# Performance work log

Hardware: AMD Instinct MI355X
Metric: run time of the kernel (lower is better)

The kernel has to match this reference:

```python
import jax, jax.numpy as jnp
import numpy as np

N_QUBITS = 14
N_LAYERS = 3
BATCH = 256


def _apply_1q(state, U, q, n):
    # state: (B, 2^n) flat; apply 2x2 gate U on qubit q.
    # U: (2,2) shared or (B,2,2) per-sample.
    B = state.shape[0]
    s = state.reshape(B, 2 ** q, 2, 2 ** (n - 1 - q))
    if U.ndim == 3:
        s = jnp.einsum('bij,bajc->baic', U, s)
    else:
        s = jnp.einsum('ij,bajc->baic', U, s)
    return s.reshape(B, -1)


def _apply_cnot(state, c, t, n):
    # CNOT: |c, t> -> |c, t xor c>. Flip target axis on the control=1 block.
    B = state.shape[0]
    a, b = (c, t) if c < t else (t, c)
    s = state.reshape(B, 2 ** a, 2, 2 ** (b - a - 1), 2, 2 ** (n - 1 - b))
    c_ax = 2 if c < t else 4
    t_ax = 4 if c < t else 2
    s0 = jax.lax.index_in_dim(s, 0, axis=c_ax, keepdims=False)
    s1 = jax.lax.index_in_dim(s, 1, axis=c_ax, keepdims=False)
    t_ax2 = t_ax if t_ax < c_ax else t_ax - 1
    s1 = jnp.flip(s1, axis=t_ax2)
    s = jnp.stack([s0, s1], axis=c_ax)
    return s.reshape(B, -1)


def _circuit(x, weights, n, L):
    # angles constrained to (-pi, pi) as in the torch wrapper
    angles = jnp.tanh(x) * jnp.float32(np.pi)  # (B, n)
    B = x.shape[0]
    state = jnp.zeros((B, 2 ** n), jnp.complex64).at[:, 0].set(1.0)
    # AngleEmbedding with RY rotations (per-sample gate matrices)
    for q in range(n):
        th = angles[:, q] * 0.5
        c, s = jnp.cos(th), jnp.sin(th)
        U = jnp.stack([jnp.stack([c, -s], -1), jnp.stack([s, c], -1)], -2)
        state = _apply_1q(state, U.astype(jnp.complex64), q, n)
    # BasicEntanglerLayers: per layer, RX(w) on each wire then CNOT ring
    for l in range(L):
        for q in range(n):
            th = weights[l, q] * 0.5
            c = jnp.cos(th).astype(jnp.complex64)
            s = jnp.sin(th).astype(jnp.complex64)
            mis = jnp.complex64(-1j) * s
            U = jnp.stack([jnp.stack([c, mis]), jnp.stack([mis, c])])
            state = _apply_1q(state, U, q, n)
        num_cnots = n if n > 2 else (1 if n == 2 else 0)
        for q in range(num_cnots):
            state = _apply_cnot(state, q, (q + 1) % n, n)
    # <Z_q> = P(q=0) - P(q=1)
    p = (jnp.abs(state) ** 2).reshape((B,) + (2,) * n)  # float32 probs
    expvals = []
    for q in range(n):
        pq = jnp.sum(p, axis=tuple(a for a in range(1, n + 1) if a != q + 1))
        expvals.append(pq[:, 0] - pq[:, 1])
    return jnp.stack(expvals, axis=-1)  # (B, n)


def setup_inputs() -> dict:
    key = jax.random.key(0)
    kx, kw = jax.random.split(key)
    x = jax.random.normal(kx, (BATCH, N_QUBITS), jnp.float32)
    # TorchLayer default init for BasicEntanglerLayers: uniform in [0, 2*pi)
    weights = jax.random.uniform(kw, (N_LAYERS, N_QUBITS), jnp.float32, 0.0, 2.0 * np.pi)
    return {"x": x, "weights": weights}


def reference(x, weights):
    return _circuit(x, weights, N_QUBITS, N_LAYERS)
```

## Files before the change

### kernel.cpp

```cpp
#include <hip/hip_runtime.h>
#include <math.h>

#define NQ 14
#define DIM (1 << NQ)
#define NT 512
#define TA 32
#define NW (NT / 64)
#define PDIM (DIM + DIM / 32)

template <int J> struct IC { static constexpr int v = J; };
template <int N, typename F>
__device__ __forceinline__ void sfor(F&& f) {
    if constexpr (N > 0) { sfor<N - 1>(f); f(IC<N - 1>{}); }
}

typedef float cf2 __attribute__((ext_vector_type(2)));

__device__ __forceinline__ cf2 pk_mul_s_swapneg(cf2 cs, cf2 a) {
    cf2 t;
    asm("v_pk_mul_f32 %0, %1, %2 op_sel:[1,1] op_sel_hi:[1,0] neg_hi:[0,1]"
        : "=v"(t) : "v"(cs), "v"(a));
    return t;
}
__device__ __forceinline__ cf2 pk_fma_c(cf2 cs, cf2 a, cf2 b) {
    cf2 d;
    asm("v_pk_fma_f32 %0, %1, %2, %3 op_sel:[0,0,0] op_sel_hi:[0,1,1]"
        : "=v"(d) : "v"(cs), "v"(a), "v"(b));
    return d;
}

struct St {
    cf2 a0, a1, a2, a3, a4, a5, a6, a7, a8, a9, a10, a11, a12, a13, a14, a15,
        a16, a17, a18, a19, a20, a21, a22, a23, a24, a25, a26, a27, a28, a29, a30, a31;
};
template <int J> __device__ __forceinline__ cf2& amp(St& s);
#define AMP_GET(J) template <> __device__ __forceinline__ cf2& amp<J>(St& s) { return s.a##J; }
AMP_GET(0)  AMP_GET(1)  AMP_GET(2)  AMP_GET(3)  AMP_GET(4)  AMP_GET(5)  AMP_GET(6)  AMP_GET(7)
AMP_GET(8)  AMP_GET(9)  AMP_GET(10) AMP_GET(11) AMP_GET(12) AMP_GET(13) AMP_GET(14) AMP_GET(15)
AMP_GET(16) AMP_GET(17) AMP_GET(18) AMP_GET(19) AMP_GET(20) AMP_GET(21) AMP_GET(22) AMP_GET(23)
AMP_GET(24) AMP_GET(25) AMP_GET(26) AMP_GET(27) AMP_GET(28) AMP_GET(29) AMP_GET(30) AMP_GET(31)

__host__ __device__ constexpr int pad(int idx) { return idx + (idx >> 5); }

template <int P0, int P1, int P2, int P3, int P4>
struct Tile5 {
    static constexpr int PMASK = (1 << P0) | (1 << P1) | (1 << P2) | (1 << P3) | (1 << P4);
    static __device__ __forceinline__ int base_idx(int t) {
        int idx = 0, tb = 0;
#pragma unroll
        for (int p = 0; p < NQ; ++p)
            if (!((PMASK >> p) & 1)) { idx |= ((t >> tb) & 1) << p; ++tb; }
        return idx;
    }
    static constexpr int off(int j) {
        return ((j & 1) << P0) | (((j >> 1) & 1) << P1) | (((j >> 2) & 1) << P2) |
               (((j >> 3) & 1) << P3) | (((j >> 4) & 1) << P4);
    }
    static constexpr int poff(int j) { return pad(off(j)); }
};

using TT1 = Tile5<9, 10, 11, 12, 13>;
using TT2 = Tile5<4, 5, 6, 7, 8>;
using TT3 = Tile5<13, 0, 1, 2, 3>;

template <class T>
__device__ __forceinline__ void load_tile(const cf2* s, int pb, St& st) {
    sfor<TA>([&](auto jc) {
        constexpr int j0 = decltype(jc)::v;
        constexpr int j = (j0 >> 1) | ((j0 & 1) << 4);
        amp<j>(st) = s[pb + T::poff(j)];
    });
}
template <class T>
__device__ __forceinline__ void load_tile_fold(const cf2* s, int pbLo, int pbHi, St& st) {
    sfor<TA>([&](auto jc) {
        constexpr int j0 = decltype(jc)::v;
        constexpr int j = (j0 >> 1) | ((j0 & 1) << 4);
        amp<j>(st) = s[((j & 16) ? pbHi : pbLo) + T::poff(j)];
    });
}
template <class T, int HI>
__device__ __forceinline__ void store_half(cf2* s, int pb, St& st) {
    sfor<TA>([&](auto jc) {
        constexpr int j = decltype(jc)::v;
        if constexpr ((j >> 4) == HI) s[pb + T::poff(j)] = amp<j>(st);
    });
}

template <int LB>
__device__ __forceinline__ void g_rx(St& st, cf2 cs) {
    sfor<TA>([&](auto jc) {
        constexpr int j = decltype(jc)::v;
        if constexpr (!(j & (1 << LB))) {
            constexpr int k = j | (1 << LB);
            cf2 aj = amp<j>(st), ak = amp<k>(st);
            amp<j>(st) = pk_fma_c(cs, aj, pk_mul_s_swapneg(cs, ak));
            amp<k>(st) = pk_fma_c(cs, ak, pk_mul_s_swapneg(cs, aj));
        }
    });
}
template <int LB, int HI>
__device__ __forceinline__ void g_rx_h(St& st, cf2 cs) {
    sfor<TA>([&](auto jc) {
        constexpr int j = decltype(jc)::v;
        if constexpr (!(j & (1 << LB)) && ((j >> 4) == HI)) {
            constexpr int k = j | (1 << LB);
            cf2 aj = amp<j>(st), ak = amp<k>(st);
            amp<j>(st) = pk_fma_c(cs, aj, pk_mul_s_swapneg(cs, ak));
            amp<k>(st) = pk_fma_c(cs, ak, pk_mul_s_swapneg(cs, aj));
        }
    });
}
template <int LC, int LT, int HI>
__device__ __forceinline__ void g_cnot_h(St& st) {
    sfor<TA>([&](auto jc) {
        constexpr int j = decltype(jc)::v;
        if constexpr (((j >> LC) & 1) && !((j >> LT) & 1) && ((j >> 4) == HI)) {
            constexpr int k = j | (1 << LT);
            cf2 t = amp<j>(st);
            amp<j>(st) = amp<k>(st);
            amp<k>(st) = t;
        }
    });
}

__device__ __forceinline__ cf2 cmul(cf2 a, cf2 b) {
    cf2 r; r.x = a.x * b.x - a.y * b.y; r.y = a.x * b.y + a.y * b.x; return r;
}
__device__ __forceinline__ cf2 v_of(cf2 ry, cf2 rx, int b) {
    cf2 r;
    r.x = b ? rx.x * ry.y : rx.x * ry.x;
    r.y = b ? -(rx.y * ry.x) : -(rx.y * ry.y);
    return r;
}

__global__ void __launch_bounds__(NT) qsim_kernel(const float* __restrict__ x,
                                                  const float* __restrict__ w,
                                                  float* __restrict__ out) {
    __shared__ cf2 sSt[PDIM];
    __shared__ cf2 sCS[56];
    __shared__ float sRed[NW][NQ];

    const int tid = threadIdx.x;
    const int b = blockIdx.x;

    if (tid < 14) {
        float th = tanhf(x[b * NQ + tid]) * 1.57079632679489662f;
        cf2 v; v.x = cosf(th); v.y = sinf(th);
        sCS[tid] = v;
    } else if (tid < 56) {
        float th = w[tid - 14] * 0.5f;
        cf2 v; v.x = cosf(th); v.y = sinf(th);
        sCS[tid] = v;
    }

    const int pbT1 = pad(TT1::base_idx(tid));
    const int pbT2 = pad(TT2::base_idx(tid));
    const int pbT3 = pad(TT3::base_idx(tid));
    const int d2 = ((tid >> 4) & 1) ? 264 : 0;
    const int pbT2lo = pbT2 + d2, pbT2hi = pbT2 - d2;
    const int d3 = (tid & 1) ? 8 : 0;
    const int pbT3lo = pbT3 + d3, pbT3hi = pbT3 - d3;

    __syncthreads();

    St st;

    {
        const int t0 = tid & 1,        t1 = (tid >> 1) & 1, t2 = (tid >> 2) & 1,
                  t3 = (tid >> 3) & 1, t4 = (tid >> 4) & 1, t5 = (tid >> 5) & 1,
                  t6 = (tid >> 6) & 1, t7 = (tid >> 7) & 1, t8 = (tid >> 8) & 1;
        const int b6 = t7 ^ t8, b7 = t6 ^ t7, b8 = t5 ^ t6, b9 = t4 ^ t5;
        const int b10 = t3 ^ t4, b11 = t2 ^ t3, b12 = t1 ^ t2, b13 = t0 ^ t1;
        cf2 Pref = v_of(sCS[6], sCS[20], b6);
        Pref = cmul(Pref, v_of(sCS[7],  sCS[21], b7));
        Pref = cmul(Pref, v_of(sCS[8],  sCS[22], b8));
        Pref = cmul(Pref, v_of(sCS[9],  sCS[23], b9));
        Pref = cmul(Pref, v_of(sCS[10], sCS[24], b10));
        Pref = cmul(Pref, v_of(sCS[11], sCS[25], b11));
        Pref = cmul(Pref, v_of(sCS[12], sCS[26], b12));
        Pref = cmul(Pref, v_of(sCS[13], sCS[27], b13));
        cf2 w0[2] = { v_of(sCS[0], sCS[14], t0),     v_of(sCS[0], sCS[14], 1 ^ t0) };
        cf2 w1[2] = { v_of(sCS[1], sCS[15], t0),     v_of(sCS[1], sCS[15], 1 ^ t0) };
        cf2 v2[2] = { v_of(sCS[2], sCS[16], 0),      v_of(sCS[2], sCS[16], 1) };
        cf2 v3[2] = { v_of(sCS[3], sCS[17], 0),      v_of(sCS[3], sCS[17], 1) };
        cf2 v4[2] = { v_of(sCS[4], sCS[18], 0),      v_of(sCS[4], sCS[18], 1) };
        cf2 w5[2] = { v_of(sCS[5], sCS[19], t8),     v_of(sCS[5], sCS[19], 1 ^ t8) };
        cf2 u[4] = { cmul(v4[0], w5[0]), cmul(v4[1], w5[1]),
                     cmul(v4[1], w5[0]), cmul(v4[0], w5[1]) };
        cf2 tA[2], tB[4], tC[8], tD[16];
        sfor<2>([&](auto ic) {
            constexpr int i = decltype(ic)::v;
            tA[i] = cmul(Pref, w0[i]);
        });
        sfor<4>([&](auto ic) {
            constexpr int i = decltype(ic)::v;
            constexpr int j4 = i >> 1, j3 = i & 1;
            tB[i] = cmul(tA[j4], w1[j3 ^ j4]);
        });
        sfor<8>([&](auto ic) {
            constexpr int i = decltype(ic)::v;
            constexpr int j3 = (i >> 1) & 1, j2 = i & 1;
            tC[i] = cmul(tB[i >> 1], v2[j2 ^ j3]);
        });
        sfor<16>([&](auto ic) {
            constexpr int i = decltype(ic)::v;
            constexpr int j2 = (i >> 1) & 1, j1 = i & 1;
            tD[i] = cmul(tC[i >> 1], v3[j1 ^ j2]);
        });
        sfor<TA>([&](auto jc) {
            constexpr int j = decltype(jc)::v;
            constexpr int j0 = j & 1, j1 = (j >> 1) & 1;
            amp<j>(st) = cmul(tD[j >> 1], u[(j1 << 1) | j0]);
        });

        g_rx<4>(st, sCS[28 + 0]);
        g_rx_h<3, 0>(st, sCS[28 + 1]); g_rx_h<2, 0>(st, sCS[28 + 2]);
        g_rx_h<1, 0>(st, sCS[28 + 3]); g_rx_h<0, 0>(st, sCS[28 + 4]);
        g_cnot_h<3, 2, 0>(st); g_cnot_h<2, 1, 0>(st); g_cnot_h<1, 0, 0>(st);
        store_half<TT1, 0>(sSt, pbT1, st);
        g_rx_h<3, 1>(st, sCS[28 + 1]); g_rx_h<2, 1>(st, sCS[28 + 2]);
        g_rx_h<1, 1>(st, sCS[28 + 3]); g_rx_h<0, 1>(st, sCS[28 + 4]);
        g_cnot_h<4, 3, 1>(st); g_cnot_h<3, 2, 1>(st); g_cnot_h<2, 1, 1>(st); g_cnot_h<1, 0, 1>(st);
        store_half<TT1, 1>(sSt, pbT1, st);
    }
    __syncthreads();

#pragma unroll 1
    for (int l = 1; l < 3; ++l) {
        const int s0 = 14 + l * NQ;
        if (l == 2) {
            cf2 c0 = sCS[s0 + 0], c1 = sCS[s0 + 1], c2 = sCS[s0 + 2];
            cf2 c3 = sCS[s0 + 3], c4 = sCS[s0 + 4];
            load_tile<TT1>(sSt, pbT1, st);
            g_rx<4>(st, c0);
            g_rx_h<3,0>(st, c1); g_rx_h<2,0>(st, c2); g_rx_h<1,0>(st, c3); g_rx_h<0,0>(st, c4);
            g_cnot_h<3,2,0>(st); g_cnot_h<2,1,0>(st); g_cnot_h<1,0,0>(st);
            store_half<TT1, 0>(sSt, pbT1, st);
            g_rx_h<3,1>(st, c1); g_rx_h<2,1>(st, c2); g_rx_h<1,1>(st, c3); g_rx_h<0,1>(st, c4);
            g_cnot_h<4,3,1>(st); g_cnot_h<3,2,1>(st); g_cnot_h<2,1,1>(st); g_cnot_h<1,0,1>(st);
            store_half<TT1, 1>(sSt, pbT1, st);
            __syncthreads();
        }
        {
            cf2 c5 = sCS[s0 + 5], c6 = sCS[s0 + 6], c7 = sCS[s0 + 7];
            cf2 c8 = sCS[s0 + 8], c9 = sCS[s0 + 9];
            load_tile_fold<TT2>(sSt, pbT2lo, pbT2hi, st);
            g_rx<4>(st, c5);
            g_rx_h<3,0>(st, c6); g_rx_h<2,0>(st, c7); g_rx_h<1,0>(st, c8); g_rx_h<0,0>(st, c9);
            g_cnot_h<3,2,0>(st); g_cnot_h<2,1,0>(st); g_cnot_h<1,0,0>(st);
            store_half<TT2, 0>(sSt, pbT2, st);
            g_rx_h<3,1>(st, c6); g_rx_h<2,1>(st, c7); g_rx_h<1,1>(st, c8); g_rx_h<0,1>(st, c9);
            g_cnot_h<4,3,1>(st); g_cnot_h<3,2,1>(st); g_cnot_h<2,1,1>(st); g_cnot_h<1,0,1>(st);
            store_half<TT2, 1>(sSt, pbT2, st);
        }
        __syncthreads();
        {
            cf2 cA = sCS[s0 + 10], cB = sCS[s0 + 11], cC = sCS[s0 + 12], cD = sCS[s0 + 13];
            load_tile_fold<TT3>(sSt, pbT3lo, pbT3hi, st);
            g_rx<4>(st, cA);
            g_rx_h<3,0>(st, cB); g_rx_h<2,0>(st, cC); g_rx_h<1,0>(st, cD);
            g_cnot_h<3,2,0>(st); g_cnot_h<2,1,0>(st); g_cnot_h<1,0,0>(st);
            if (l == 1) store_half<TT3, 0>(sSt, pbT3, st);
            g_rx_h<3,1>(st, cB); g_rx_h<2,1>(st, cC); g_rx_h<1,1>(st, cD);
            g_cnot_h<4,3,1>(st); g_cnot_h<3,2,1>(st); g_cnot_h<2,1,1>(st); g_cnot_h<1,0,1>(st);
            if (l == 1) store_half<TT3, 1>(sSt, pbT3, st);
        }
        if (l == 1) __syncthreads();
    }

    float Stot = 0.f, S0 = 0.f, S1 = 0.f, S2 = 0.f, S3 = 0.f, S4 = 0.f;
    sfor<TA>([&](auto jc) {
        constexpr int j = decltype(jc)::v;
        cf2 v = amp<j>(st);
        float pj = v.x * v.x + v.y * v.y;
        Stot += pj;
        S0 += (j & 1)  ? -pj : pj;
        S1 += (j & 2)  ? -pj : pj;
        S2 += (j & 4)  ? -pj : pj;
        S3 += (j & 8)  ? -pj : pj;
        S4 += (j & 16) ? -pj : pj;
    });
    float ev[NQ];
    ev[0] = S0; ev[10] = S4; ev[11] = S3; ev[12] = S2; ev[13] = S1;
#pragma unroll
    for (int q = 1; q <= 9; ++q)
        ev[q] = ((tid >> (9 - q)) & 1) ? -Stot : Stot;

#pragma unroll
    for (int q = 0; q < NQ; ++q) {
#pragma unroll
        for (int o = 32; o > 0; o >>= 1) ev[q] += __shfl_down(ev[q], o);
    }
    const int wv = tid >> 6, ln = tid & 63;
    if (ln == 0) {
#pragma unroll
        for (int q = 0; q < NQ; ++q) sRed[wv][q] = ev[q];
    }
    __syncthreads();
    if (tid < NQ) {
        float acc = 0.f;
#pragma unroll
        for (int k = 0; k < NW; ++k) acc += sRed[k][tid];
        out[b * NQ + tid] = acc;
    }
}

extern "C" void kernel_launch(void* const* d_in, const int* in_sizes, int n_in,
                              void* d_out, int out_size, void* d_ws, size_t ws_size,
                              hipStream_t stream) {
    const float* x = (const float*)d_in[0];
    const float* w = (const float*)d_in[1];
    float* out = (float*)d_out;
    qsim_kernel<<<256, NT, 0, stream>>>(x, w, out);
}
```

Baseline: 71.00 us.

## Fuse last layer via cross-lane RX gates and fold final CNOT ring into measurement

Unrolls the layer loop and restructures layer three. Most of its RX gates are applied in the TT3 tile, with the qubits that live on lanes handled by DPP and ds_swizzle exchanges. The remaining gates run in a new TP4 tile. The final CNOT ring is never applied to the state; its effect is folded into parity-based sign patterns when computing the Z expectations. This removes one full shared-memory tile pass and its barrier, at the cost of cross-lane shuffle instructions and more complex index and sign logic.

```diff
diff --git a/kernel.cpp b/kernel.cpp
--- a/kernel.cpp
+++ b/kernel.cpp
@@ -62,6 +62,7 @@
 using TT1 = Tile5<9, 10, 11, 12, 13>;
 using TT2 = Tile5<4, 5, 6, 7, 8>;
 using TT3 = Tile5<13, 0, 1, 2, 3>;
+using TP4 = Tile5<8, 9, 10, 11, 12>;
 
 template <class T>
 __device__ __forceinline__ void load_tile(const cf2* s, int pb, St& st) {
@@ -108,6 +109,34 @@
             cf2 aj = amp<j>(st), ak = amp<k>(st);
             amp<j>(st) = pk_fma_c(cs, aj, pk_mul_s_swapneg(cs, ak));
             amp<k>(st) = pk_fma_c(cs, ak, pk_mul_s_swapneg(cs, aj));
+        }
+    });
+}
+template <int CTRL, int HI>
+__device__ __forceinline__ void g_rx_lane_dpp(St& st, cf2 cs) {
+    sfor<TA>([&](auto jc) {
+        constexpr int j = decltype(jc)::v;
+        if constexpr ((j >> 4) == HI) {
+            cf2 a = amp<j>(st);
+            int px = __builtin_amdgcn_update_dpp(__float_as_int(a.x), __float_as_int(a.x),
+                                                 CTRL, 0xF, 0xF, false);
+            int py = __builtin_amdgcn_update_dpp(__float_as_int(a.y), __float_as_int(a.y),
+                                                 CTRL, 0xF, 0xF, false);
+            cf2 p; p.x = __int_as_float(px); p.y = __int_as_float(py);
+            amp<j>(st) = pk_fma_c(cs, a, pk_mul_s_swapneg(cs, p));
+        }
+    });
+}
+template <int PAT, int HI>
+__device__ __forceinline__ void g_rx_lane_swz(St& st, cf2 cs) {
+    sfor<TA>([&](auto jc) {
+        constexpr int j = decltype(jc)::v;
+        if constexpr ((j >> 4) == HI) {
+            cf2 a = amp<j>(st);
+            int px = __builtin_amdgcn_ds_swizzle(__float_as_int(a.x), PAT);
+            int py = __builtin_amdgcn_ds_swizzle(__float_as_int(a.y), PAT);
+            cf2 p; p.x = __int_as_float(px); p.y = __int_as_float(py);
+            amp<j>(st) = pk_fma_c(cs, a, pk_mul_s_swapneg(cs, p));
         }
     });
 }
@@ -157,6 +186,7 @@
     const int pbT1 = pad(TT1::base_idx(tid));
     const int pbT2 = pad(TT2::base_idx(tid));
     const int pbT3 = pad(TT3::base_idx(tid));
+    const int pbT4 = pad(TP4::base_idx(tid));
     const int d2 = ((tid >> 4) & 1) ? 264 : 0;
     const int pbT2lo = pbT2 + d2, pbT2hi = pbT2 - d2;
     const int d3 = (tid & 1) ? 8 : 0;
@@ -226,83 +256,110 @@
     }
     __syncthreads();
 
-#pragma unroll 1
-    for (int l = 1; l < 3; ++l) {
-        const int s0 = 14 + l * NQ;
-        if (l == 2) {
-            cf2 c0 = sCS[s0 + 0], c1 = sCS[s0 + 1], c2 = sCS[s0 + 2];
-            cf2 c3 = sCS[s0 + 3], c4 = sCS[s0 + 4];
-            load_tile<TT1>(sSt, pbT1, st);
-            g_rx<4>(st, c0);
-            g_rx_h<3,0>(st, c1); g_rx_h<2,0>(st, c2); g_rx_h<1,0>(st, c3); g_rx_h<0,0>(st, c4);
-            g_cnot_h<3,2,0>(st); g_cnot_h<2,1,0>(st); g_cnot_h<1,0,0>(st);
-            store_half<TT1, 0>(sSt, pbT1, st);
-            g_rx_h<3,1>(st, c1); g_rx_h<2,1>(st, c2); g_rx_h<1,1>(st, c3); g_rx_h<0,1>(st, c4);
-            g_cnot_h<4,3,1>(st); g_cnot_h<3,2,1>(st); g_cnot_h<2,1,1>(st); g_cnot_h<1,0,1>(st);
-            store_half<TT1, 1>(sSt, pbT1, st);
-            __syncthreads();
-        }
-        {
-            cf2 c5 = sCS[s0 + 5], c6 = sCS[s0 + 6], c7 = sCS[s0 + 7];
-            cf2 c8 = sCS[s0 + 8], c9 = sCS[s0 + 9];
-            load_tile_fold<TT2>(sSt, pbT2lo, pbT2hi, st);
-            g_rx<4>(st, c5);
-            g_rx_h<3,0>(st, c6); g_rx_h<2,0>(st, c7); g_rx_h<1,0>(st, c8); g_rx_h<0,0>(st, c9);
-            g_cnot_h<3,2,0>(st); g_cnot_h<2,1,0>(st); g_cnot_h<1,0,0>(st);
-            store_half<TT2, 0>(sSt, pbT2, st);
-            g_rx_h<3,1>(st, c6); g_rx_h<2,1>(st, c7); g_rx_h<1,1>(st, c8); g_rx_h<0,1>(st, c9);
-            g_cnot_h<4,3,1>(st); g_cnot_h<3,2,1>(st); g_cnot_h<2,1,1>(st); g_cnot_h<1,0,1>(st);
-            store_half<TT2, 1>(sSt, pbT2, st);
+    {
+        cf2 c5 = sCS[28 + 5], c6 = sCS[28 + 6], c7 = sCS[28 + 7];
+        cf2 c8 = sCS[28 + 8], c9 = sCS[28 + 9];
+        load_tile_fold<TT2>(sSt, pbT2lo, pbT2hi, st);
+        g_rx<4>(st, c5);
+        g_rx_h<3,0>(st, c6); g_rx_h<2,0>(st, c7); g_rx_h<1,0>(st, c8); g_rx_h<0,0>(st, c9);
+        g_cnot_h<3,2,0>(st); g_cnot_h<2,1,0>(st); g_cnot_h<1,0,0>(st);
+        store_half<TT2, 0>(sSt, pbT2, st);
+        g_rx_h<3,1>(st, c6); g_rx_h<2,1>(st, c7); g_rx_h<1,1>(st, c8); g_rx_h<0,1>(st, c9);
+        g_cnot_h<4,3,1>(st); g_cnot_h<3,2,1>(st); g_cnot_h<2,1,1>(st); g_cnot_h<1,0,1>(st);
+        store_half<TT2, 1>(sSt, pbT2, st);
+    }
+    __syncthreads();
+
+    {
+        cf2 cA = sCS[28 + 10], cB = sCS[28 + 11], cC = sCS[28 + 12], cD = sCS[28 + 13];
+        load_tile_fold<TT3>(sSt, pbT3lo, pbT3hi, st);
+        g_rx<4>(st, cA);
+        g_rx_h<3,0>(st, cB); g_rx_h<2,0>(st, cC); g_rx_h<1,0>(st, cD);
+        g_cnot_h<3,2,0>(st); g_cnot_h<2,1,0>(st); g_cnot_h<1,0,0>(st);
+        g_rx_h<3,1>(st, cB); g_rx_h<2,1>(st, cC); g_rx_h<1,1>(st, cD);
+        g_cnot_h<4,3,1>(st); g_cnot_h<3,2,1>(st); g_cnot_h<2,1,1>(st); g_cnot_h<1,0,1>(st);
+        g_rx<4>(st, sCS[42 + 10]);
+        g_rx_h<3,0>(st, sCS[42 + 11]); g_rx_h<2,0>(st, sCS[42 + 12]);
+        g_rx_h<1,0>(st, sCS[42 + 13]); g_rx_h<0,0>(st, sCS[42 + 0]);
+        g_rx_lane_dpp<0xB1, 0>(st, sCS[42 + 9]);
+        g_rx_lane_dpp<0x4E, 0>(st, sCS[42 + 8]);
+        g_rx_lane_swz<0x101F, 0>(st, sCS[42 + 7]);
+        g_rx_lane_swz<0x201F, 0>(st, sCS[42 + 6]);
+        store_half<TT3, 0>(sSt, pbT3, st);
+        g_rx_h<3,1>(st, sCS[42 + 11]); g_rx_h<2,1>(st, sCS[42 + 12]);
+        g_rx_h<1,1>(st, sCS[42 + 13]); g_rx_h<0,1>(st, sCS[42 + 0]);
+        g_rx_lane_dpp<0xB1, 1>(st, sCS[42 + 9]);
+        g_rx_lane_dpp<0x4E, 1>(st, sCS[42 + 8]);
+        g_rx_lane_swz<0x101F, 1>(st, sCS[42 + 7]);
+        g_rx_lane_swz<0x201F, 1>(st, sCS[42 + 6]);
+        store_half<TT3, 1>(sSt, pbT3, st);
+    }
+    __syncthreads();
+
+    {
+        load_tile<TP4>(sSt, pbT4, st);
+        g_rx<4>(st, sCS[42 + 1]);
+        g_rx<3>(st, sCS[42 + 2]); g_rx<2>(st, sCS[42 + 3]);
+        g_rx<1>(st, sCS[42 + 4]); g_rx<0>(st, sCS[42 + 5]);
+
+        float A1 = 0.f, A2 = 0.f, A3 = 0.f, A4 = 0.f, A5 = 0.f;
+        sfor<TA>([&](auto jc) {
+            constexpr int j = decltype(jc)::v;
+            cf2 v = amp<j>(st);
+            float pj = v.x * v.x + v.y * v.y;
+            constexpr int s1 = (j >> 4) & 1;
+            constexpr int s2 = s1 ^ ((j >> 3) & 1);
+            constexpr int s3 = s2 ^ ((j >> 2) & 1);
+            constexpr int s4 = s3 ^ ((j >> 1) & 1);
+            constexpr int s5 = s4 ^ (j & 1);
+            A1 += s1 ? -pj : pj;
+            A2 += s2 ? -pj : pj;
+            A3 += s3 ? -pj : pj;
+            A4 += s4 ? -pj : pj;
+            A5 += s5 ? -pj : pj;
+        });
+        const int t0 = tid & 1,        t1 = (tid >> 1) & 1, t2 = (tid >> 2) & 1,
+                  t3 = (tid >> 3) & 1, t4 = (tid >> 4) & 1, t5 = (tid >> 5) & 1,
+                  t6 = (tid >> 6) & 1, t7 = (tid >> 7) & 1, t8 = (tid >> 8) & 1;
+        const int g6 = t8 ^ t7;
+        const int g7 = g6 ^ t6;
+        const int g8 = g7 ^ t5, g9 = g8 ^ t4, g10 = g9 ^ t3;
+        const int g11 = g10 ^ t2, g12 = g11 ^ t1, g13 = g12 ^ t0;
+        const int g0 = g13 ^ t8;
+
+        float ev[NQ];
+        ev[0]  = g0 ? -A5 : A5;
+        ev[1]  = t8 ? -A1 : A1;
+        ev[2]  = t8 ? -A2 : A2;
+        ev[3]  = t8 ? -A3 : A3;
+        ev[4]  = t8 ? -A4 : A4;
+        ev[5]  = t8 ? -A5 : A5;
+        ev[6]  = g6 ? -A5 : A5;
+        ev[7]  = g7 ? -A5 : A5;
+        ev[8]  = g8 ? -A5 : A5;
+        ev[9]  = g9 ? -A5 : A5;
+        ev[10] = g10 ? -A5 : A5;
+        ev[11] = g11 ? -A5 : A5;
+        ev[12] = g12 ? -A5 : A5;
+        ev[13] = g13 ? -A5 : A5;
+
+#pragma unroll
+        for (int q = 0; q < NQ; ++q) {
+#pragma unroll
+            for (int o = 32; o > 0; o >>= 1) ev[q] += __shfl_down(ev[q], o);
+        }
+        const int wv = tid >> 6, ln = tid & 63;
+        if (ln == 0) {
+#pragma unroll
+            for (int q = 0; q < NQ; ++q) sRed[wv][q] = ev[q];
         }
         __syncthreads();
-        {
-            cf2 cA = sCS[s0 + 10], cB = sCS[s0 + 11], cC = sCS[s0 + 12], cD = sCS[s0 + 13];
-            load_tile_fold<TT3>(sSt, pbT3lo, pbT3hi, st);
-            g_rx<4>(st, cA);
-            g_rx_h<3,0>(st, cB); g_rx_h<2,0>(st, cC); g_rx_h<1,0>(st, cD);
-            g_cnot_h<3,2,0>(st); g_cnot_h<2,1,0>(st); g_cnot_h<1,0,0>(st);
-            if (l == 1) store_half<TT3, 0>(sSt, pbT3, st);
-            g_rx_h<3,1>(st, cB); g_rx_h<2,1>(st, cC); g_rx_h<1,1>(st, cD);
-            g_cnot_h<4,3,1>(st); g_cnot_h<3,2,1>(st); g_cnot_h<2,1,1>(st); g_cnot_h<1,0,1>(st);
-            if (l == 1) store_half<TT3, 1>(sSt, pbT3, st);
-        }
-        if (l == 1) __syncthreads();
-    }
-
-    float Stot = 0.f, S0 = 0.f, S1 = 0.f, S2 = 0.f, S3 = 0.f, S4 = 0.f;
-    sfor<TA>([&](auto jc) {
-        constexpr int j = decltype(jc)::v;
-        cf2 v = amp<j>(st);
-        float pj = v.x * v.x + v.y * v.y;
-        Stot += pj;
-        S0 += (j & 1)  ? -pj : pj;
-        S1 += (j & 2)  ? -pj : pj;
-        S2 += (j & 4)  ? -pj : pj;
-        S3 += (j & 8)  ? -pj : pj;
-        S4 += (j & 16) ? -pj : pj;
-    });
-    float ev[NQ];
-    ev[0] = S0; ev[10] = S4; ev[11] = S3; ev[12] = S2; ev[13] = S1;
-#pragma unroll
-    for (int q = 1; q <= 9; ++q)
-        ev[q] = ((tid >> (9 - q)) & 1) ? -Stot : Stot;
-
-#pragma unroll
-    for (int q = 0; q < NQ; ++q) {
-#pragma unroll
-        for (int o = 32; o > 0; o >>= 1) ev[q] += __shfl_down(ev[q], o);
-    }
-    const int wv = tid >> 6, ln = tid & 63;
-    if (ln == 0) {
-#pragma unroll
-        for (int q = 0; q < NQ; ++q) sRed[wv][q] = ev[q];
-    }
-    __syncthreads();
-    if (tid < NQ) {
-        float acc = 0.f;
-#pragma unroll
-        for (int k = 0; k < NW; ++k) acc += sRed[k][tid];
-        out[b * NQ + tid] = acc;
+        if (tid < NQ) {
+            float acc = 0.f;
+#pragma unroll
+            for (int k = 0; k < NW; ++k) acc += sRed[k][tid];
+            out[b * NQ + tid] = acc;
+        }
     }
 }
 
```

Measured after the change: 72.06 us. Within noise of the previous version (+1.5%).

## Eliminate final layer's state passes by commuting CNOT ring into measurement

Applied to the files above, without the earlier changes.

The last entangler layer is no longer applied as separate load/compute/store passes. Its RX gates are folded into the earlier tile passes, one cross-lane qubit uses DPP lane swaps, and the final CNOT ring is absorbed into parity-based sign patterns when computing the Z expectations. This removes a full TT1 pass plus a store/sync round over shared memory, which cuts LDS traffic and barriers. In exchange it uses a remapped thread-to-index layout for tile 2, adds DPP operations, and relies on intricate parity logic that must be exactly right.

```diff
diff --git a/kernel.cpp b/kernel.cpp
--- a/kernel.cpp
+++ b/kernel.cpp
@@ -58,19 +58,25 @@
     }
     static constexpr int poff(int j) { return pad(off(j)); }
 };
+template <int P0, int P1, int P2, int P3, int P4,
+          int Q0, int Q1, int Q2, int Q3, int Q4, int Q5, int Q6, int Q7, int Q8>
+struct Tile5Q {
+    static __device__ __forceinline__ int base_idx(int t) {
+        return (((t >> 0) & 1) << Q0) | (((t >> 1) & 1) << Q1) | (((t >> 2) & 1) << Q2) |
+               (((t >> 3) & 1) << Q3) | (((t >> 4) & 1) << Q4) | (((t >> 5) & 1) << Q5) |
+               (((t >> 6) & 1) << Q6) | (((t >> 7) & 1) << Q7) | (((t >> 8) & 1) << Q8);
+    }
+    static constexpr int off(int j) {
+        return ((j & 1) << P0) | (((j >> 1) & 1) << P1) | (((j >> 2) & 1) << P2) |
+               (((j >> 3) & 1) << P3) | (((j >> 4) & 1) << P4);
+    }
+    static constexpr int poff(int j) { return pad(off(j)); }
+};
 
 using TT1 = Tile5<9, 10, 11, 12, 13>;
-using TT2 = Tile5<4, 5, 6, 7, 8>;
+using TT2Q = Tile5Q<4, 5, 6, 7, 8,  9, 0, 1, 2, 3, 10, 11, 12, 13>;
 using TT3 = Tile5<13, 0, 1, 2, 3>;
 
-template <class T>
-__device__ __forceinline__ void load_tile(const cf2* s, int pb, St& st) {
-    sfor<TA>([&](auto jc) {
-        constexpr int j0 = decltype(jc)::v;
-        constexpr int j = (j0 >> 1) | ((j0 & 1) << 4);
-        amp<j>(st) = s[pb + T::poff(j)];
-    });
-}
 template <class T>
 __device__ __forceinline__ void load_tile_fold(const cf2* s, int pbLo, int pbHi, St& st) {
     sfor<TA>([&](auto jc) {
@@ -109,6 +115,19 @@
             amp<j>(st) = pk_fma_c(cs, aj, pk_mul_s_swapneg(cs, ak));
             amp<k>(st) = pk_fma_c(cs, ak, pk_mul_s_swapneg(cs, aj));
         }
+    });
+}
+template <int CTRL>
+__device__ __forceinline__ void g_rx_lane_dpp(St& st, cf2 cs) {
+    sfor<TA>([&](auto jc) {
+        constexpr int j = decltype(jc)::v;
+        cf2 a = amp<j>(st);
+        int px = __builtin_amdgcn_update_dpp(__float_as_int(a.x), __float_as_int(a.x),
+                                             CTRL, 0xF, 0xF, false);
+        int py = __builtin_amdgcn_update_dpp(__float_as_int(a.y), __float_as_int(a.y),
+                                             CTRL, 0xF, 0xF, false);
+        cf2 p; p.x = __int_as_float(px); p.y = __int_as_float(py);
+        amp<j>(st) = pk_fma_c(cs, a, pk_mul_s_swapneg(cs, p));
     });
 }
 template <int LC, int LT, int HI>
@@ -155,9 +174,9 @@
     }
 
     const int pbT1 = pad(TT1::base_idx(tid));
-    const int pbT2 = pad(TT2::base_idx(tid));
+    const int pbT2 = pad(TT2Q::base_idx(tid));
     const int pbT3 = pad(TT3::base_idx(tid));
-    const int d2 = ((tid >> 4) & 1) ? 264 : 0;
+    const int d2 = (tid & 1) ? 264 : 0;
     const int pbT2lo = pbT2 + d2, pbT2hi = pbT2 - d2;
     const int d3 = (tid & 1) ? 8 : 0;
     const int pbT3lo = pbT3 + d3, pbT3hi = pbT3 - d3;
@@ -218,91 +237,115 @@
         g_rx_h<3, 0>(st, sCS[28 + 1]); g_rx_h<2, 0>(st, sCS[28 + 2]);
         g_rx_h<1, 0>(st, sCS[28 + 3]); g_rx_h<0, 0>(st, sCS[28 + 4]);
         g_cnot_h<3, 2, 0>(st); g_cnot_h<2, 1, 0>(st); g_cnot_h<1, 0, 0>(st);
+        g_rx_h<3, 0>(st, sCS[42 + 1]); g_rx_h<2, 0>(st, sCS[42 + 2]);
+        g_rx_h<1, 0>(st, sCS[42 + 3]);
         store_half<TT1, 0>(sSt, pbT1, st);
         g_rx_h<3, 1>(st, sCS[28 + 1]); g_rx_h<2, 1>(st, sCS[28 + 2]);
         g_rx_h<1, 1>(st, sCS[28 + 3]); g_rx_h<0, 1>(st, sCS[28 + 4]);
         g_cnot_h<4, 3, 1>(st); g_cnot_h<3, 2, 1>(st); g_cnot_h<2, 1, 1>(st); g_cnot_h<1, 0, 1>(st);
+        g_rx_h<3, 1>(st, sCS[42 + 1]); g_rx_h<2, 1>(st, sCS[42 + 2]);
+        g_rx_h<1, 1>(st, sCS[42 + 3]);
         store_half<TT1, 1>(sSt, pbT1, st);
     }
     __syncthreads();
 
-#pragma unroll 1
-    for (int l = 1; l < 3; ++l) {
-        const int s0 = 14 + l * NQ;
-        if (l == 2) {
-            cf2 c0 = sCS[s0 + 0], c1 = sCS[s0 + 1], c2 = sCS[s0 + 2];
-            cf2 c3 = sCS[s0 + 3], c4 = sCS[s0 + 4];
-            load_tile<TT1>(sSt, pbT1, st);
-            g_rx<4>(st, c0);
-            g_rx_h<3,0>(st, c1); g_rx_h<2,0>(st, c2); g_rx_h<1,0>(st, c3); g_rx_h<0,0>(st, c4);
-            g_cnot_h<3,2,0>(st); g_cnot_h<2,1,0>(st); g_cnot_h<1,0,0>(st);
-            store_half<TT1, 0>(sSt, pbT1, st);
-            g_rx_h<3,1>(st, c1); g_rx_h<2,1>(st, c2); g_rx_h<1,1>(st, c3); g_rx_h<0,1>(st, c4);
-            g_cnot_h<4,3,1>(st); g_cnot_h<3,2,1>(st); g_cnot_h<2,1,1>(st); g_cnot_h<1,0,1>(st);
-            store_half<TT1, 1>(sSt, pbT1, st);
-            __syncthreads();
-        }
-        {
-            cf2 c5 = sCS[s0 + 5], c6 = sCS[s0 + 6], c7 = sCS[s0 + 7];
-            cf2 c8 = sCS[s0 + 8], c9 = sCS[s0 + 9];
-            load_tile_fold<TT2>(sSt, pbT2lo, pbT2hi, st);
-            g_rx<4>(st, c5);
-            g_rx_h<3,0>(st, c6); g_rx_h<2,0>(st, c7); g_rx_h<1,0>(st, c8); g_rx_h<0,0>(st, c9);
-            g_cnot_h<3,2,0>(st); g_cnot_h<2,1,0>(st); g_cnot_h<1,0,0>(st);
-            store_half<TT2, 0>(sSt, pbT2, st);
-            g_rx_h<3,1>(st, c6); g_rx_h<2,1>(st, c7); g_rx_h<1,1>(st, c8); g_rx_h<0,1>(st, c9);
-            g_cnot_h<4,3,1>(st); g_cnot_h<3,2,1>(st); g_cnot_h<2,1,1>(st); g_cnot_h<1,0,1>(st);
-            store_half<TT2, 1>(sSt, pbT2, st);
+    {
+        cf2 c5 = sCS[28 + 5], c6 = sCS[28 + 6], c7 = sCS[28 + 7];
+        cf2 c8 = sCS[28 + 8], c9 = sCS[28 + 9];
+        cf2 e4 = sCS[42 + 4], e5 = sCS[42 + 5], e6 = sCS[42 + 6];
+        cf2 e7 = sCS[42 + 7], e8 = sCS[42 + 8];
+        load_tile_fold<TT2Q>(sSt, pbT2lo, pbT2hi, st);
+        g_rx<4>(st, c5);
+        g_rx_lane_dpp<0xB1>(st, e4);
+        g_rx_h<3,0>(st, c6); g_rx_h<2,0>(st, c7); g_rx_h<1,0>(st, c8); g_rx_h<0,0>(st, c9);
+        g_cnot_h<3,2,0>(st); g_cnot_h<2,1,0>(st); g_cnot_h<1,0,0>(st);
+        g_rx_h<3,1>(st, c6); g_rx_h<2,1>(st, c7); g_rx_h<1,1>(st, c8); g_rx_h<0,1>(st, c9);
+        g_cnot_h<4,3,1>(st); g_cnot_h<3,2,1>(st); g_cnot_h<2,1,1>(st); g_cnot_h<1,0,1>(st);
+        g_rx<4>(st, e5);
+        g_rx_h<3,0>(st, e6); g_rx_h<2,0>(st, e7); g_rx_h<1,0>(st, e8);
+        store_half<TT2Q, 0>(sSt, pbT2, st);
+        g_rx_h<3,1>(st, e6); g_rx_h<2,1>(st, e7); g_rx_h<1,1>(st, e8);
+        store_half<TT2Q, 1>(sSt, pbT2, st);
+    }
+    __syncthreads();
+
+    {
+        cf2 cA = sCS[28 + 10], cB = sCS[28 + 11], cC = sCS[28 + 12], cD = sCS[28 + 13];
+        cf2 eA = sCS[42 + 10], eB = sCS[42 + 11], eC = sCS[42 + 12], eD = sCS[42 + 13];
+        cf2 e9 = sCS[42 + 9],  e0 = sCS[42 + 0];
+        load_tile_fold<TT3>(sSt, pbT3lo, pbT3hi, st);
+        g_rx<4>(st, cA);
+        g_rx_lane_dpp<0xB1>(st, e9);
+        g_rx_h<3,0>(st, cB); g_rx_h<2,0>(st, cC); g_rx_h<1,0>(st, cD);
+        g_cnot_h<3,2,0>(st); g_cnot_h<2,1,0>(st); g_cnot_h<1,0,0>(st);
+        g_rx_h<3,1>(st, cB); g_rx_h<2,1>(st, cC); g_rx_h<1,1>(st, cD);
+        g_cnot_h<4,3,1>(st); g_cnot_h<3,2,1>(st); g_cnot_h<2,1,1>(st); g_cnot_h<1,0,1>(st);
+        g_rx<4>(st, eA);
+        g_rx_h<3,0>(st, eB); g_rx_h<2,0>(st, eC); g_rx_h<1,0>(st, eD); g_rx_h<0,0>(st, e0);
+        g_rx_h<3,1>(st, eB); g_rx_h<2,1>(st, eC); g_rx_h<1,1>(st, eD); g_rx_h<0,1>(st, e0);
+    }
+
+    {
+        float Aa = 0.f, Ab = 0.f, Ac = 0.f, Ad = 0.f, Ae = 0.f, Af = 0.f;
+        sfor<TA>([&](auto jc) {
+            constexpr int j = decltype(jc)::v;
+            cf2 v = amp<j>(st);
+            float pj = v.x * v.x + v.y * v.y;
+            constexpr int j0 = j & 1, j1 = (j >> 1) & 1, j2 = (j >> 2) & 1,
+                          j3 = (j >> 3) & 1, j4 = (j >> 4) & 1;
+            constexpr int sa = j0;
+            constexpr int sb = j0 ^ j4;
+            constexpr int sc = sb ^ j3;
+            constexpr int sd = sc ^ j2;
+            constexpr int se = sd ^ j1;
+            constexpr int sf = se ^ j0;
+            Aa += sa ? -pj : pj;
+            Ab += sb ? -pj : pj;
+            Ac += sc ? -pj : pj;
+            Ad += sd ? -pj : pj;
+            Ae += se ? -pj : pj;
+            Af += sf ? -pj : pj;
+        });
+        const int t0 = tid & 1,        t1 = (tid >> 1) & 1, t2 = (tid >> 2) & 1,
+                  t3 = (tid >> 3) & 1, t4 = (tid >> 4) & 1, t5 = (tid >> 5) & 1,
+                  t6 = (tid >> 6) & 1, t7 = (tid >> 7) & 1, t8 = (tid >> 8) & 1;
+        const int T1 = t8,      T2 = T1 ^ t7, T3 = T2 ^ t6, T4 = T3 ^ t5;
+        const int T5 = T4 ^ t4, T6 = T5 ^ t3, T7 = T6 ^ t2, T8 = T7 ^ t1;
+        const int T9 = T8 ^ t0;
+
+        float ev[NQ];
+        ev[0]  = T9 ? -Af : Af;
+        ev[1]  = T1 ? -Aa : Aa;
+        ev[2]  = T2 ? -Aa : Aa;
+        ev[3]  = T3 ? -Aa : Aa;
+        ev[4]  = T4 ? -Aa : Aa;
+        ev[5]  = T5 ? -Aa : Aa;
+        ev[6]  = T6 ? -Aa : Aa;
+        ev[7]  = T7 ? -Aa : Aa;
+        ev[8]  = T8 ? -Aa : Aa;
+        ev[9]  = T9 ? -Aa : Aa;
+        ev[10] = T9 ? -Ab : Ab;
+        ev[11] = T9 ? -Ac : Ac;
+        ev[12] = T9 ? -Ad : Ad;
+        ev[13] = T9 ? -Ae : Ae;
+
+#pragma unroll
+        for (int q = 0; q < NQ; ++q) {
+#pragma unroll
+            for (int o = 32; o > 0; o >>= 1) ev[q] += __shfl_down(ev[q], o);
+        }
+        const int wv = tid >> 6, ln = tid & 63;
+        if (ln == 0) {
+#pragma unroll
+            for (int q = 0; q < NQ; ++q) sRed[wv][q] = ev[q];
         }
         __syncthreads();
-        {
-            cf2 cA = sCS[s0 + 10], cB = sCS[s0 + 11], cC = sCS[s0 + 12], cD = sCS[s0 + 13];
-            load_tile_fold<TT3>(sSt, pbT3lo, pbT3hi, st);
-            g_rx<4>(st, cA);
-            g_rx_h<3,0>(st, cB); g_rx_h<2,0>(st, cC); g_rx_h<1,0>(st, cD);
-            g_cnot_h<3,2,0>(st); g_cnot_h<2,1,0>(st); g_cnot_h<1,0,0>(st);
-            if (l == 1) store_half<TT3, 0>(sSt, pbT3, st);
-            g_rx_h<3,1>(st, cB); g_rx_h<2,1>(st, cC); g_rx_h<1,1>(st, cD);
-            g_cnot_h<4,3,1>(st); g_cnot_h<3,2,1>(st); g_cnot_h<2,1,1>(st); g_cnot_h<1,0,1>(st);
-            if (l == 1) store_half<TT3, 1>(sSt, pbT3, st);
-        }
-        if (l == 1) __syncthreads();
-    }
-
-    float Stot = 0.f, S0 = 0.f, S1 = 0.f, S2 = 0.f, S3 = 0.f, S4 = 0.f;
-    sfor<TA>([&](auto jc) {
-        constexpr int j = decltype(jc)::v;
-        cf2 v = amp<j>(st);
-        float pj = v.x * v.x + v.y * v.y;
-        Stot += pj;
-        S0 += (j & 1)  ? -pj : pj;
-        S1 += (j & 2)  ? -pj : pj;
-        S2 += (j & 4)  ? -pj : pj;
-        S3 += (j & 8)  ? -pj : pj;
-        S4 += (j & 16) ? -pj : pj;
-    });
-    float ev[NQ];
-    ev[0] = S0; ev[10] = S4; ev[11] = S3; ev[12] = S2; ev[13] = S1;
-#pragma unroll
-    for (int q = 1; q <= 9; ++q)
-        ev[q] = ((tid >> (9 - q)) & 1) ? -Stot : Stot;
-
-#pragma unroll
-    for (int q = 0; q < NQ; ++q) {
-#pragma unroll
-        for (int o = 32; o > 0; o >>= 1) ev[q] += __shfl_down(ev[q], o);
-    }
-    const int wv = tid >> 6, ln = tid & 63;
-    if (ln == 0) {
-#pragma unroll
-        for (int q = 0; q < NQ; ++q) sRed[wv][q] = ev[q];
-    }
-    __syncthreads();
-    if (tid < NQ) {
-        float acc = 0.f;
-#pragma unroll
-        for (int k = 0; k < NW; ++k) acc += sRed[k][tid];
-        out[b * NQ + tid] = acc;
+        if (tid < NQ) {
+            float acc = 0.f;
+#pragma unroll
+            for (int k = 0; k < NW; ++k) acc += sRed[k][tid];
+            out[b * NQ + tid] = acc;
+        }
     }
 }
 
```

Measured after the change: 69.58 us. -2.0%, faster.
